# Kernel optimization log

Hardware: AMD Instinct MI355X
Metric: run time of the kernel (lower is better)

The kernel has to match this reference:

```python
import jax, jax.numpy as jnp
import numpy as np

N_NODES = 100000
N_EDGES = 1200000
D_FEAT = 64


def setup_inputs() -> dict:
    key = jax.random.key(0)
    k1, k2, k3 = jax.random.split(key, 3)
    x = jax.random.normal(k1, (N_NODES, D_FEAT), dtype=jnp.float32)
    edge_index = jax.random.randint(k2, (2, N_EDGES), 0, N_NODES, dtype=jnp.int64)
    edge_weight = jax.random.uniform(k3, (N_EDGES, 1), dtype=jnp.float32)
    return {"x": x, "edge_index": edge_index, "edge_weight": edge_weight}


def reference(x, edge_index, edge_weight):
    # flow = source_to_target: j = edge_index[0] (source), i = edge_index[1] (target)
    src, dst = edge_index[0], edge_index[1]
    # message: x_j  (gather along node_dim=-2)
    msg = x[src]                       # [E, D]
    # aggregate: scatter-'sum' with edge_weight scaling
    msg = msg * edge_weight            # [E, D]
    out = jax.ops.segment_sum(msg, dst, num_segments=N_NODES)  # [N, D]
    # update: identity
    return out
```

## Files before the change

### kernel.cpp

```cpp
#include <hip/hip_runtime.h>
#include <hip/hip_bf16.h>


constexpr int D_FEAT        = 64;
constexpr int BIN_SHIFT     = 6;
constexpr int NODES_PER_BIN = 1 << BIN_SHIFT;
constexpr int NBINS_MAX     = 2048;
constexpr int BIN_CAP       = 1024;
constexpr int EPB           = 4096;
constexpr int OVF_CAP       = 32768;

__device__ __forceinline__ int wave_incl_scan(int v, int lane) {
    #pragma unroll
    for (int d = 1; d < 64; d <<= 1) {
        int t = __shfl_up(v, d);
        if (lane >= d) v += t;
    }
    return v;
}

__device__ __forceinline__ unsigned short f32_to_bf16_rn(float f) {
    unsigned int u = __float_as_uint(f);
    u += 0x7FFFu + ((u >> 16) & 1u);
    return (unsigned short)(u >> 16);
}

__global__ __launch_bounds__(1024) void mp_partition(
    const int* __restrict__ src, const int* __restrict__ dst,
    const float* __restrict__ w, const float* __restrict__ x,
    ushort* __restrict__ xb, int n4,
    int*  __restrict__ gcnt,
    int2* __restrict__ payload,
    int*  __restrict__ ovf_cnt, int4* __restrict__ ovf,
    int n_edges, int nbins)
{
    __shared__ int cnt[NBINS_MAX];
    __shared__ int start[NBINS_MAX];
    __shared__ int cur[NBINS_MAX];
    __shared__ int gbase[NBINS_MAX];
    __shared__ unsigned short binof[EPB];
    __shared__ int2 sorted[EPB];
    __shared__ int wsum[16];

    const int t    = threadIdx.x;
    const int lane = t & 63;
    const int wid  = t >> 6;
    const int base = blockIdx.x * EPB;
    const int nblk = min(EPB, n_edges - base);

    for (int i = blockIdx.x * 1024 + t; i < n4; i += gridDim.x * 1024) {
        const float4 v = reinterpret_cast<const float4*>(x)[i];
        ushort4 o;
        o.x = f32_to_bf16_rn(v.x);
        o.y = f32_to_bf16_rn(v.y);
        o.z = f32_to_bf16_rn(v.z);
        o.w = f32_to_bf16_rn(v.w);
        reinterpret_cast<ushort4*>(xb)[i] = o;
    }

    cnt[t] = 0;
    cnt[t + 1024] = 0;
    __syncthreads();

    const int i4 = (base >> 2) + t;
    int4 d4 = make_int4(0, 0, 0, 0);
    bool have = (i4 * 4 < n_edges);
    if (have) {
        d4 = reinterpret_cast<const int4*>(dst)[i4];
        atomicAdd(&cnt[d4.x >> BIN_SHIFT], 1);
        atomicAdd(&cnt[d4.y >> BIN_SHIFT], 1);
        atomicAdd(&cnt[d4.z >> BIN_SHIFT], 1);
        atomicAdd(&cnt[d4.w >> BIN_SHIFT], 1);
    }
    __syncthreads();

    const int b2 = t * 2;
    const int c0 = (b2     < nbins) ? cnt[b2]     : 0;
    const int c1 = (b2 + 1 < nbins) ? cnt[b2 + 1] : 0;
    const int l  = c0 + c1;
    const int incl = wave_incl_scan(l, lane);
    if (lane == 63) wsum[wid] = incl;
    __syncthreads();
    int woff = 0;
    #pragma unroll
    for (int k = 0; k < 16; ++k) woff += (k < wid) ? wsum[k] : 0;
    const int excl = woff + incl - l;
    if (b2 < nbins) {
        start[b2] = excl;
        cur[b2]   = excl;
        if (c0 > 0) gbase[b2] = atomicAdd(&gcnt[b2], c0);
    }
    if (b2 + 1 < nbins) {
        start[b2 + 1] = excl + c0;
        cur[b2 + 1]   = excl + c0;
        if (c1 > 0) gbase[b2 + 1] = atomicAdd(&gcnt[b2 + 1], c1);
    }
    __syncthreads();

    if (have) {
        const int4   s4 = reinterpret_cast<const int4*>(src)[i4];
        const float4 w4 = reinterpret_cast<const float4*>(w)[i4];
        const int   dd[4] = {d4.x, d4.y, d4.z, d4.w};
        const int   ss[4] = {s4.x, s4.y, s4.z, s4.w};
        const float ww[4] = {w4.x, w4.y, w4.z, w4.w};
        #pragma unroll
        for (int j = 0; j < 4; ++j) {
            const int b   = dd[j] >> BIN_SHIFT;
            const int low = dd[j] & (NODES_PER_BIN - 1);
            const int p   = atomicAdd(&cur[b], 1);
            sorted[p] = make_int2((low << 20) | ss[j], __float_as_int(ww[j]));
            binof[p]  = (unsigned short)b;
        }
    }
    __syncthreads();

    #pragma unroll
    for (int k = 0; k < EPB / 1024; ++k) {
        const int i = k * 1024 + t;
        if (i >= nblk) break;
        const int b    = binof[i];
        const int idx  = i - start[b];
        const int gpos = gbase[b] + idx;
        const int2 e   = sorted[i];
        if (gpos < BIN_CAP) {
            payload[(size_t)b * BIN_CAP + gpos] = e;
        } else {
            const int op = atomicAdd(ovf_cnt, 1);
            if (op < OVF_CAP)
                ovf[op] = make_int4((b << BIN_SHIFT) + (e.x >> 20),
                                    e.x & 0xFFFFF, e.y, 0);
        }
    }
}

__global__ __launch_bounds__(512) void mp_bin_gather(
    const ushort* __restrict__ xb,
    const float*  __restrict__ x,
    const int*  __restrict__ gcnt,
    const int2* __restrict__ payload,
    const int*  __restrict__ ovf_cnt, const int4* __restrict__ ovf,
    float* __restrict__ out, int n_nodes)
{
    __shared__ int2 sraw[BIN_CAP];
    __shared__ int2 sedge[BIN_CAP];
    __shared__ int ncnt[NODES_PER_BIN];
    __shared__ int nstart[NODES_PER_BIN + 1];
    __shared__ int ncur[NODES_PER_BIN];

    const int b    = blockIdx.x;
    const int t    = threadIdx.x;
    const int lane = t & 63;
    const int wid  = t >> 6;
    const int sub  = lane >> 3;
    const int fq   = lane & 7;
    const int fg   = fq * 8;

    const int m = min(gcnt[b], BIN_CAP);
    const int2* pl = payload + (size_t)b * BIN_CAP;

    if (t < NODES_PER_BIN) ncnt[t] = 0;
    __syncthreads();

    for (int i = t; i < m; i += 512) {
        const int2 e = pl[i];
        sraw[i] = e;
        atomicAdd(&ncnt[e.x >> 20], 1);
    }
    __syncthreads();

    if (t < 64) {
        const int a0 = ncnt[t];
        const int s0 = wave_incl_scan(a0, t);
        nstart[t] = s0 - a0;
        if (t == 63) nstart[64] = s0;
    }
    __syncthreads();
    if (t < NODES_PER_BIN) ncur[t] = nstart[t];
    __syncthreads();

    for (int i = t; i < m; i += 512) {
        const int2 e = sraw[i];
        const int p  = atomicAdd(&ncur[e.x >> 20], 1);
        sedge[p] = e;
    }
    __syncthreads();

    const int novf = *ovf_cnt;

    const int n    = wid * 8 + sub;
    const int node = (b << BIN_SHIFT) + n;
    const int s0 = nstart[n];
    const int s1 = nstart[n + 1];

    float a0 = 0.f, a1 = 0.f, a2 = 0.f, a3 = 0.f;
    float a4 = 0.f, a5 = 0.f, a6 = 0.f, a7 = 0.f;

    int e = s0;
    for (; e + 4 <= s1; e += 4) {
        const int2 p0 = sedge[e];
        const int2 p1 = sedge[e + 1];
        const int2 p2 = sedge[e + 2];
        const int2 p3 = sedge[e + 3];
        const uint4 x0 = *reinterpret_cast<const uint4*>(
            xb + (size_t)(p0.x & 0xFFFFF) * D_FEAT + fg);
        const uint4 x1 = *reinterpret_cast<const uint4*>(
            xb + (size_t)(p1.x & 0xFFFFF) * D_FEAT + fg);
        const uint4 x2 = *reinterpret_cast<const uint4*>(
            xb + (size_t)(p2.x & 0xFFFFF) * D_FEAT + fg);
        const uint4 x3 = *reinterpret_cast<const uint4*>(
            xb + (size_t)(p3.x & 0xFFFFF) * D_FEAT + fg);
        const float w0 = __int_as_float(p0.y);
        const float w1 = __int_as_float(p1.y);
        const float w2 = __int_as_float(p2.y);
        const float w3 = __int_as_float(p3.y);
        a0 = fmaf(__uint_as_float(x0.x << 16),         w0, a0);
        a1 = fmaf(__uint_as_float(x0.x & 0xFFFF0000u), w0, a1);
        a2 = fmaf(__uint_as_float(x0.y << 16),         w0, a2);
        a3 = fmaf(__uint_as_float(x0.y & 0xFFFF0000u), w0, a3);
        a4 = fmaf(__uint_as_float(x0.z << 16),         w0, a4);
        a5 = fmaf(__uint_as_float(x0.z & 0xFFFF0000u), w0, a5);
        a6 = fmaf(__uint_as_float(x0.w << 16),         w0, a6);
        a7 = fmaf(__uint_as_float(x0.w & 0xFFFF0000u), w0, a7);
        a0 = fmaf(__uint_as_float(x1.x << 16),         w1, a0);
        a1 = fmaf(__uint_as_float(x1.x & 0xFFFF0000u), w1, a1);
        a2 = fmaf(__uint_as_float(x1.y << 16),         w1, a2);
        a3 = fmaf(__uint_as_float(x1.y & 0xFFFF0000u), w1, a3);
        a4 = fmaf(__uint_as_float(x1.z << 16),         w1, a4);
        a5 = fmaf(__uint_as_float(x1.z & 0xFFFF0000u), w1, a5);
        a6 = fmaf(__uint_as_float(x1.w << 16),         w1, a6);
        a7 = fmaf(__uint_as_float(x1.w & 0xFFFF0000u), w1, a7);
        a0 = fmaf(__uint_as_float(x2.x << 16),         w2, a0);
        a1 = fmaf(__uint_as_float(x2.x & 0xFFFF0000u), w2, a1);
        a2 = fmaf(__uint_as_float(x2.y << 16),         w2, a2);
        a3 = fmaf(__uint_as_float(x2.y & 0xFFFF0000u), w2, a3);
        a4 = fmaf(__uint_as_float(x2.z << 16),         w2, a4);
        a5 = fmaf(__uint_as_float(x2.z & 0xFFFF0000u), w2, a5);
        a6 = fmaf(__uint_as_float(x2.w << 16),         w2, a6);
        a7 = fmaf(__uint_as_float(x2.w & 0xFFFF0000u), w2, a7);
        a0 = fmaf(__uint_as_float(x3.x << 16),         w3, a0);
        a1 = fmaf(__uint_as_float(x3.x & 0xFFFF0000u), w3, a1);
        a2 = fmaf(__uint_as_float(x3.y << 16),         w3, a2);
        a3 = fmaf(__uint_as_float(x3.y & 0xFFFF0000u), w3, a3);
        a4 = fmaf(__uint_as_float(x3.z << 16),         w3, a4);
        a5 = fmaf(__uint_as_float(x3.z & 0xFFFF0000u), w3, a5);
        a6 = fmaf(__uint_as_float(x3.w << 16),         w3, a6);
        a7 = fmaf(__uint_as_float(x3.w & 0xFFFF0000u), w3, a7);
    }
    for (; e + 2 <= s1; e += 2) {
        const int2 p0 = sedge[e];
        const int2 p1 = sedge[e + 1];
        const uint4 x0 = *reinterpret_cast<const uint4*>(
            xb + (size_t)(p0.x & 0xFFFFF) * D_FEAT + fg);
        const uint4 x1 = *reinterpret_cast<const uint4*>(
            xb + (size_t)(p1.x & 0xFFFFF) * D_FEAT + fg);
        const float w0 = __int_as_float(p0.y);
        const float w1 = __int_as_float(p1.y);
        a0 = fmaf(__uint_as_float(x0.x << 16),         w0, a0);
        a1 = fmaf(__uint_as_float(x0.x & 0xFFFF0000u), w0, a1);
        a2 = fmaf(__uint_as_float(x0.y << 16),         w0, a2);
        a3 = fmaf(__uint_as_float(x0.y & 0xFFFF0000u), w0, a3);
        a4 = fmaf(__uint_as_float(x0.z << 16),         w0, a4);
        a5 = fmaf(__uint_as_float(x0.z & 0xFFFF0000u), w0, a5);
        a6 = fmaf(__uint_as_float(x0.w << 16),         w0, a6);
        a7 = fmaf(__uint_as_float(x0.w & 0xFFFF0000u), w0, a7);
        a0 = fmaf(__uint_as_float(x1.x << 16),         w1, a0);
        a1 = fmaf(__uint_as_float(x1.x & 0xFFFF0000u), w1, a1);
        a2 = fmaf(__uint_as_float(x1.y << 16),         w1, a2);
        a3 = fmaf(__uint_as_float(x1.y & 0xFFFF0000u), w1, a3);
        a4 = fmaf(__uint_as_float(x1.z << 16),         w1, a4);
        a5 = fmaf(__uint_as_float(x1.z & 0xFFFF0000u), w1, a5);
        a6 = fmaf(__uint_as_float(x1.w << 16),         w1, a6);
        a7 = fmaf(__uint_as_float(x1.w & 0xFFFF0000u), w1, a7);
    }
    if (e < s1) {
        const int2 p = sedge[e];
        const uint4 xv = *reinterpret_cast<const uint4*>(
            xb + (size_t)(p.x & 0xFFFFF) * D_FEAT + fg);
        const float ww = __int_as_float(p.y);
        a0 = fmaf(__uint_as_float(xv.x << 16),         ww, a0);
        a1 = fmaf(__uint_as_float(xv.x & 0xFFFF0000u), ww, a1);
        a2 = fmaf(__uint_as_float(xv.y << 16),         ww, a2);
        a3 = fmaf(__uint_as_float(xv.y & 0xFFFF0000u), ww, a3);
        a4 = fmaf(__uint_as_float(xv.z << 16),         ww, a4);
        a5 = fmaf(__uint_as_float(xv.z & 0xFFFF0000u), ww, a5);
        a6 = fmaf(__uint_as_float(xv.w << 16),         ww, a6);
        a7 = fmaf(__uint_as_float(xv.w & 0xFFFF0000u), ww, a7);
    }

    if (node < n_nodes) {
        if (novf > 0) {
            const int lim = min(novf, OVF_CAP);
            for (int j = 0; j < lim; ++j) {
                const int4 o = ovf[j];
                if (o.x == node) {
                    const float* xr = x + (size_t)o.y * D_FEAT + fg;
                    const float ww = __int_as_float(o.z);
                    a0 = fmaf(xr[0], ww, a0); a1 = fmaf(xr[1], ww, a1);
                    a2 = fmaf(xr[2], ww, a2); a3 = fmaf(xr[3], ww, a3);
                    a4 = fmaf(xr[4], ww, a4); a5 = fmaf(xr[5], ww, a5);
                    a6 = fmaf(xr[6], ww, a6); a7 = fmaf(xr[7], ww, a7);
                }
            }
        }
        float* orow = out + (size_t)node * D_FEAT + fg;
        *reinterpret_cast<float4*>(orow)     = make_float4(a0, a1, a2, a3);
        *reinterpret_cast<float4*>(orow + 4) = make_float4(a4, a5, a6, a7);
    }
}

__global__ __launch_bounds__(256) void mp_scatter_atomic(
    const float* __restrict__ x, const int* __restrict__ src,
    const int* __restrict__ dst, const float* __restrict__ w,
    float* __restrict__ out, int n_edges)
{
    const int gtid = blockIdx.x * blockDim.x + threadIdx.x;
    const int edge = gtid >> 6;
    const int lane = threadIdx.x & 63;
    if (edge >= n_edges) return;
    const int s = src[edge];
    const int d = dst[edge];
    const float ww = w[edge];
    atomicAdd(&out[(size_t)d * D_FEAT + lane], x[(size_t)s * D_FEAT + lane] * ww);
}

extern "C" void kernel_launch(void* const* d_in, const int* in_sizes, int n_in,
                              void* d_out, int out_size, void* d_ws, size_t ws_size,
                              hipStream_t stream)
{
    const float* x          = (const float*)d_in[0];
    const int*   edge_index = (const int*)d_in[1];
    const float* w          = (const float*)d_in[2];
    float*       out        = (float*)d_out;

    const int n_edges = in_sizes[1] / 2;
    const int n_nodes = in_sizes[0] / D_FEAT;
    const int* src = edge_index;
    const int* dst = edge_index + n_edges;

    const int nbins = (n_nodes + NODES_PER_BIN - 1) >> BIN_SHIFT;

    int*    gcnt    = (int*)d_ws;
    int*    ovf_cnt = gcnt + NBINS_MAX;
    int4*   ovf     = (int4*)(gcnt + NBINS_MAX + 64);
    int2*   payload = (int2*)(ovf + OVF_CAP);
    ushort* xb      = (ushort*)(payload + (size_t)nbins * BIN_CAP);
    const size_t need = (size_t)(NBINS_MAX + 64) * 4 + (size_t)OVF_CAP * 16
                      + (size_t)nbins * BIN_CAP * 8
                      + (size_t)n_nodes * D_FEAT * 2;

    const bool ok = (ws_size >= need) && (nbins <= NBINS_MAX) && ((n_edges & 3) == 0)
                 && ((n_nodes * D_FEAT) % 4 == 0);

    if (ok) {
        hipMemsetAsync(gcnt, 0, (size_t)(NBINS_MAX + 64) * 4, stream);
        const int n4 = n_nodes * D_FEAT / 4;
        const int g1 = (n_edges + EPB - 1) / EPB;
        mp_partition<<<g1, 1024, 0, stream>>>(src, dst, w, x, xb, n4,
                                              gcnt, payload, ovf_cnt, ovf,
                                              n_edges, nbins);
        mp_bin_gather<<<nbins, 512, 0, stream>>>(xb, x, gcnt, payload,
                                                 ovf_cnt, ovf, out, n_nodes);
        return;
    }

    hipMemsetAsync(d_out, 0, (size_t)out_size * sizeof(float), stream);
    const int grid = (int)(((size_t)n_edges * 64 + 255) / 256);
    mp_scatter_atomic<<<grid, 256, 0, stream>>>(x, src, dst, w, out, n_edges);
}
```

Before: 127.8 us.

## Replace in-block counting sort with fixed per-node LDS slots and local overflow

```diff
diff --git a/kernel.cpp b/kernel.cpp
--- a/kernel.cpp
+++ b/kernel.cpp
@@ -9,6 +9,9 @@
 constexpr int BIN_CAP       = 1024;
 constexpr int EPB           = 4096;
 constexpr int OVF_CAP       = 32768;
+constexpr int SLOT_CAP      = 32;
+constexpr int SLOT_PITCH    = SLOT_CAP + 1;
+constexpr int LOVF_CAP      = 256;
 
 __device__ __forceinline__ int wave_incl_scan(int v, int lane) {
     #pragma unroll
@@ -138,14 +141,13 @@
     const float*  __restrict__ x,
     const int*  __restrict__ gcnt,
     const int2* __restrict__ payload,
-    const int*  __restrict__ ovf_cnt, const int4* __restrict__ ovf,
+    int* __restrict__ ovf_cnt, int4* __restrict__ ovf,
     float* __restrict__ out, int n_nodes)
 {
-    __shared__ int2 sraw[BIN_CAP];
-    __shared__ int2 sedge[BIN_CAP];
-    __shared__ int ncnt[NODES_PER_BIN];
-    __shared__ int nstart[NODES_PER_BIN + 1];
-    __shared__ int ncur[NODES_PER_BIN];
+    __shared__ int2 slots[NODES_PER_BIN * SLOT_PITCH];
+    __shared__ int  scnt[NODES_PER_BIN];
+    __shared__ int2 lovf[LOVF_CAP];
+    __shared__ int  lcnt;
 
     const int b    = blockIdx.x;
     const int t    = threadIdx.x;
@@ -155,52 +157,50 @@
     const int fq   = lane & 7;
     const int fg   = fq * 8;
 
+    if (t < NODES_PER_BIN) scnt[t] = 0;
+    if (t == 0) lcnt = 0;
+    __syncthreads();
+
     const int m = min(gcnt[b], BIN_CAP);
     const int2* pl = payload + (size_t)b * BIN_CAP;
 
-    if (t < NODES_PER_BIN) ncnt[t] = 0;
-    __syncthreads();
-
+    bool wrote_govf = false;
     for (int i = t; i < m; i += 512) {
         const int2 e = pl[i];
-        sraw[i] = e;
-        atomicAdd(&ncnt[e.x >> 20], 1);
-    }
-    __syncthreads();
-
-    if (t < 64) {
-        const int a0 = ncnt[t];
-        const int s0 = wave_incl_scan(a0, t);
-        nstart[t] = s0 - a0;
-        if (t == 63) nstart[64] = s0;
-    }
-    __syncthreads();
-    if (t < NODES_PER_BIN) ncur[t] = nstart[t];
-    __syncthreads();
-
-    for (int i = t; i < m; i += 512) {
-        const int2 e = sraw[i];
-        const int p  = atomicAdd(&ncur[e.x >> 20], 1);
-        sedge[p] = e;
-    }
-    __syncthreads();
-
-    const int novf = *ovf_cnt;
+        const int node = e.x >> 20;
+        const int pos = atomicAdd(&scnt[node], 1);
+        if (pos < SLOT_CAP) {
+            slots[node * SLOT_PITCH + pos] = e;
+        } else {
+            const int lp = atomicAdd(&lcnt, 1);
+            if (lp < LOVF_CAP) {
+                lovf[lp] = e;
+            } else {
+                const int op = atomicAdd(ovf_cnt, 1);
+                if (op < OVF_CAP)
+                    ovf[op] = make_int4((b << BIN_SHIFT) + node,
+                                        e.x & 0xFFFFF, e.y, 0);
+                wrote_govf = true;
+            }
+        }
+    }
+    if (wrote_govf) __threadfence();
+    __syncthreads();
 
     const int n    = wid * 8 + sub;
     const int node = (b << BIN_SHIFT) + n;
-    const int s0 = nstart[n];
-    const int s1 = nstart[n + 1];
+    const int cnt  = min(scnt[n], SLOT_CAP);
+    const int2* sp = slots + n * SLOT_PITCH;
 
     float a0 = 0.f, a1 = 0.f, a2 = 0.f, a3 = 0.f;
     float a4 = 0.f, a5 = 0.f, a6 = 0.f, a7 = 0.f;
 
-    int e = s0;
-    for (; e + 4 <= s1; e += 4) {
-        const int2 p0 = sedge[e];
-        const int2 p1 = sedge[e + 1];
-        const int2 p2 = sedge[e + 2];
-        const int2 p3 = sedge[e + 3];
+    int e = 0;
+    for (; e + 4 <= cnt; e += 4) {
+        const int2 p0 = sp[e];
+        const int2 p1 = sp[e + 1];
+        const int2 p2 = sp[e + 2];
+        const int2 p3 = sp[e + 3];
         const uint4 x0 = *reinterpret_cast<const uint4*>(
             xb + (size_t)(p0.x & 0xFFFFF) * D_FEAT + fg);
         const uint4 x1 = *reinterpret_cast<const uint4*>(
@@ -246,34 +246,8 @@
         a6 = fmaf(__uint_as_float(x3.w << 16),         w3, a6);
         a7 = fmaf(__uint_as_float(x3.w & 0xFFFF0000u), w3, a7);
     }
-    for (; e + 2 <= s1; e += 2) {
-        const int2 p0 = sedge[e];
-        const int2 p1 = sedge[e + 1];
-        const uint4 x0 = *reinterpret_cast<const uint4*>(
-            xb + (size_t)(p0.x & 0xFFFFF) * D_FEAT + fg);
-        const uint4 x1 = *reinterpret_cast<const uint4*>(
-            xb + (size_t)(p1.x & 0xFFFFF) * D_FEAT + fg);
-        const float w0 = __int_as_float(p0.y);
-        const float w1 = __int_as_float(p1.y);
-        a0 = fmaf(__uint_as_float(x0.x << 16),         w0, a0);
-        a1 = fmaf(__uint_as_float(x0.x & 0xFFFF0000u), w0, a1);
-        a2 = fmaf(__uint_as_float(x0.y << 16),         w0, a2);
-        a3 = fmaf(__uint_as_float(x0.y & 0xFFFF0000u), w0, a3);
-        a4 = fmaf(__uint_as_float(x0.z << 16),         w0, a4);
-        a5 = fmaf(__uint_as_float(x0.z & 0xFFFF0000u), w0, a5);
-        a6 = fmaf(__uint_as_float(x0.w << 16),         w0, a6);
-        a7 = fmaf(__uint_as_float(x0.w & 0xFFFF0000u), w0, a7);
-        a0 = fmaf(__uint_as_float(x1.x << 16),         w1, a0);
-        a1 = fmaf(__uint_as_float(x1.x & 0xFFFF0000u), w1, a1);
-        a2 = fmaf(__uint_as_float(x1.y << 16),         w1, a2);
-        a3 = fmaf(__uint_as_float(x1.y & 0xFFFF0000u), w1, a3);
-        a4 = fmaf(__uint_as_float(x1.z << 16),         w1, a4);
-        a5 = fmaf(__uint_as_float(x1.z & 0xFFFF0000u), w1, a5);
-        a6 = fmaf(__uint_as_float(x1.w << 16),         w1, a6);
-        a7 = fmaf(__uint_as_float(x1.w & 0xFFFF0000u), w1, a7);
-    }
-    if (e < s1) {
-        const int2 p = sedge[e];
+    for (; e < cnt; ++e) {
+        const int2 p = sp[e];
         const uint4 xv = *reinterpret_cast<const uint4*>(
             xb + (size_t)(p.x & 0xFFFFF) * D_FEAT + fg);
         const float ww = __int_as_float(p.y);
@@ -287,7 +261,26 @@
         a7 = fmaf(__uint_as_float(xv.w & 0xFFFF0000u), ww, a7);
     }
 
+    const int ll = min(lcnt, LOVF_CAP);
+    for (int j = 0; j < ll; ++j) {
+        const int2 p = lovf[j];
+        if ((p.x >> 20) == n) {
+            const uint4 xv = *reinterpret_cast<const uint4*>(
+                xb + (size_t)(p.x & 0xFFFFF) * D_FEAT + fg);
+            const float ww = __int_as_float(p.y);
+            a0 = fmaf(__uint_as_float(xv.x << 16),         ww, a0);
+            a1 = fmaf(__uint_as_float(xv.x & 0xFFFF0000u), ww, a1);
+            a2 = fmaf(__uint_as_float(xv.y << 16),         ww, a2);
+            a3 = fmaf(__uint_as_float(xv.y & 0xFFFF0000u), ww, a3);
+            a4 = fmaf(__uint_as_float(xv.z << 16),         ww, a4);
+            a5 = fmaf(__uint_as_float(xv.z & 0xFFFF0000u), ww, a5);
+            a6 = fmaf(__uint_as_float(xv.w << 16),         ww, a6);
+            a7 = fmaf(__uint_as_float(xv.w & 0xFFFF0000u), ww, a7);
+        }
+    }
+
     if (node < n_nodes) {
+        const int novf = *ovf_cnt;
         if (novf > 0) {
             const int lim = min(novf, OVF_CAP);
             for (int j = 0; j < lim; ++j) {
```

Result: no change. 128.1 us (+0.2%).
